# Optimization experiments

Hardware: AMD Instinct MI355X
Metric: run time of the kernel (lower is better)

## Reference

```python
import jax, jax.numpy as jnp
import numpy as np

K = 1024          # num_embeddings (static for segment_sum)
D = 256           # embedding_dim
B, H, W = 32, 64, 64
DECAY = 0.99
EPS = 1e-05
BETA = 0.25


def setup_inputs() -> dict:
    key = jax.random.key(0)
    k1, k2 = jax.random.split(key)
    z = jax.random.normal(k1, (B, D, H, W), dtype=jnp.float32)
    embedding = jax.random.normal(k2, (K, D), dtype=jnp.float32)
    ema_cluster_size = jnp.zeros((K,), dtype=jnp.float32)
    ema_embedding = embedding.copy()
    return {"z": z, "embedding": embedding,
            "ema_cluster_size": ema_cluster_size,
            "ema_embedding": ema_embedding}


def reference(z, embedding, ema_cluster_size, ema_embedding):
    b, d, h, w = z.shape
    # (B, D, H, W) -> (B*H*W, D)
    z_flat = jnp.transpose(z, (0, 2, 3, 1)).reshape(-1, d)
    # squared L2 distances to each code: ||z||^2 - 2 z.E^T + ||E||^2  -> (N, K)
    dist = (jnp.sum(z_flat * z_flat, axis=1, keepdims=True)
            - 2.0 * (z_flat @ embedding.T)
            + jnp.sum(embedding * embedding, axis=1))
    encoding_indices = jnp.argmin(dist, axis=1)                 # (N,)
    # one-hot @ embedding == gather
    quantized = embedding[encoding_indices]                     # (N, D)
    quantized = jnp.transpose(quantized.reshape(b, h, w, d), (0, 3, 1, 2))
    # EMA buffer updates (encodings.sum(0) and encodings.T @ z_flat as segment sums)
    counts = jax.ops.segment_sum(jnp.ones_like(encoding_indices, dtype=z.dtype),
                                 encoding_indices, num_segments=K)
    dw = jax.ops.segment_sum(z_flat, encoding_indices, num_segments=K)
    new_cluster_size = DECAY * ema_cluster_size + (1.0 - DECAY) * counts
    new_ema_embedding = DECAY * ema_embedding + (1.0 - DECAY) * dw
    # straight-through estimator
    quantized_ste = z + jax.lax.stop_gradient(quantized - z)
    commitment_loss = BETA * jnp.mean(jnp.square(z - jax.lax.stop_gradient(quantized_ste)))
    return (quantized_ste, commitment_loss, encoding_indices,
            new_cluster_size, new_ema_embedding)
```

## Files before the change

### kernel.cpp

```cpp
#include <hip/hip_runtime.h>

#define KC 1024
#define DD 256
#define NP 131072
#define HWSZ 4096
#define TOTZ 33554432

#define OUT_Q    0
#define OUT_LOSS 33554432
#define OUT_IDX  33554433
#define OUT_CS   33685505
#define OUT_EMA  33686529

#define WS_IDX    0
#define WS_COUNTS 131072
#define WS_RCNT   132096
#define WS_LOSSP  132352
#define WS_ENORM  132608
#define WS_RLIST  133632
#define WS_EAUG   264704
#define WS_NEED_FLOATS (WS_EAUG + 393216)

#define MARGIN 0.0625f
#define RTILE 16

typedef __attribute__((ext_vector_type(8))) short bf16x8;
typedef __attribute__((ext_vector_type(4))) float f32x4;

__device__ inline unsigned short f2bf_rne(float x) {
    unsigned u = __float_as_uint(x);
    unsigned r = u + 0x7FFFu + ((u >> 16) & 1u);
    return (unsigned short)(r >> 16);
}
__device__ inline float bf2f(unsigned short h) {
    return __uint_as_float(((unsigned)h) << 16);
}
__device__ inline unsigned long long packkey(float d, int c) {
    unsigned u = __float_as_uint(d);
    u = (u & 0x80000000u) ? ~u : (u | 0x80000000u);
    return (((unsigned long long)u) << 32) | (unsigned)c;
}

__global__ __launch_bounds__(256) void enorm_kernel(const float* __restrict__ emb,
                                                    float* __restrict__ enorm) {
    const int k = blockIdx.x;
    float v = emb[k * DD + threadIdx.x];
    v *= v;
    #pragma unroll
    for (int off = 32; off > 0; off >>= 1) v += __shfl_down(v, off);
    __shared__ float red[4];
    if ((threadIdx.x & 63) == 0) red[threadIdx.x >> 6] = v;
    __syncthreads();
    if (threadIdx.x == 0) enorm[k] = (red[0] + red[1]) + (red[2] + red[3]);
}

__global__ __launch_bounds__(256) void convert_emb_kernel(
    const float* __restrict__ emb, unsigned short* __restrict__ eaug)
{
    const int blk = blockIdx.x;
    const int cc = blk >> 3, ksp = blk & 7;
    const int ks = ksp + ((ksp >= 4) ? 4 : 0);
    const int mode = (ks >= 8);
    unsigned short* outp = eaug + (size_t)(cc * 12 + ks) * 8192;
    #pragma unroll
    for (int i = 0; i < 4; ++i) {
        const int f = i * 256 + threadIdx.x;
        const int kc = f >> 9, nt = (f >> 6) & 7, lane = f & 63;
        const int q = lane >> 4, col = lane & 15;
        const int n = cc * 128 + nt * 16 + col;
        const int k0 = ((ks * 64) & 255) + kc * 32 + q * 8;
        const float* src = emb + (size_t)n * 256 + k0;
        unsigned short v[8];
        #pragma unroll
        for (int j = 0; j < 8; ++j) {
            const float x = src[j];
            const unsigned short h = f2bf_rne(x);
            v[j] = mode ? f2bf_rne(x - bf2f(h)) : h;
        }
        *(uint4*)(outp + (size_t)f * 8) = *(uint4*)v;
    }
}

__global__ __launch_bounds__(512, 2) void gemm_argmin_kernel(
    const float* __restrict__ z, const unsigned short* __restrict__ eaug,
    const float* __restrict__ enorm, int* __restrict__ idx_out,
    float* __restrict__ idx_out_f, float* __restrict__ counts,
    int* __restrict__ rcnt, int* __restrict__ rlist)
{
    __shared__ float smem[39296];
    unsigned short* aS = (unsigned short*)smem;
    float* dumpB = smem + 32768;
    float* dumpS = smem + 32768 + 2176;
    int*   dumpI = (int*)(smem + 32768 + 4352);
    const int t = threadIdx.x, w = t >> 6, lane = t & 63;
    const int q = lane >> 4, col = lane & 15;
    const int pt = blockIdx.x;

    #pragma unroll 2
    for (int jj0 = 0; jj0 < 8; ++jj0) {
        const int jj = jj0 * 512 + t;
        const int kslot = jj >> 10;
        const int r = jj & 1023;
        const int kc = r >> 9, mt = (r >> 6) & 7, lf = r & 63;
        const int qq = lf >> 4, cl = lf & 15;
        const int p = pt * 128 + mt * 16 + cl;
        const int b = p >> 12, hw = p & 4095;
        const int k0 = kslot * 64 + kc * 32 + qq * 8;
        const float* src = z + (size_t)b * 1048576 + (size_t)k0 * 4096 + hw;
        unsigned short vh[8], vm[8];
        #pragma unroll
        for (int i = 0; i < 8; ++i) {
            const float x = src[i * 4096];
            const unsigned short h = f2bf_rne(x);
            vh[i] = h;
            vm[i] = f2bf_rne(x - bf2f(h));
        }
        const int off = kc * 4096 + mt * 512 + lf * 8;
        *(uint4*)(aS + kslot * 8192 + off) = *(uint4*)vh;
        *(uint4*)(aS + (4 + kslot) * 8192 + off) = *(uint4*)vm;
    }
    __syncthreads();

#define MFMA_SET(BREG, KCI)                                                   \
    {                                                                         \
        bf16x8 af[8];                                                         \
        _Pragma("unroll")                                                     \
        for (int mi = 0; mi < 8; ++mi)                                        \
            af[mi] = *(const bf16x8*)(aS + slabH * 8192 + (KCI) * 4096        \
                                      + mi * 512 + lane * 8);                 \
        __builtin_amdgcn_s_setprio(1);                                        \
        _Pragma("unroll")                                                     \
        for (int mi = 0; mi < 8; ++mi)                                        \
            _Pragma("unroll")                                                 \
            for (int ni = 0; ni < 4; ++ni)                                    \
                acc[mi][ni] = __builtin_amdgcn_mfma_f32_16x16x32_bf16(        \
                    af[mi], BREG[ni], acc[mi][ni], 0, 0, 0);                  \
        __builtin_amdgcn_s_setprio(0);                                        \
        if (s < 4) {                                                          \
            _Pragma("unroll")                                                 \
            for (int mi = 0; mi < 8; ++mi)                                    \
                af[mi] = *(const bf16x8*)(aS + (4 + slabH) * 8192             \
                                          + (KCI) * 4096 + mi * 512           \
                                          + lane * 8);                        \
            __builtin_amdgcn_s_setprio(1);                                    \
            _Pragma("unroll")                                                 \
            for (int mi = 0; mi < 8; ++mi)                                    \
                _Pragma("unroll")                                             \
                for (int ni = 0; ni < 4; ++ni)                                \
                    acc[mi][ni] = __builtin_amdgcn_mfma_f32_16x16x32_bf16(    \
                        af[mi], BREG[ni], acc[mi][ni], 0, 0, 0);              \
            __builtin_amdgcn_s_setprio(0);                                    \
        }                                                                     \
    }

    #pragma unroll 1
    for (int g = 0; g < 2; ++g) {
        const int ccg = g * 4 + (w >> 1);
        const int nqh = w & 1;
        const int nbase = g * 512 + w * 64;
        const unsigned short* eb = eaug + (size_t)ccg * 98304 + nqh * 2048
                                 + (size_t)lane * 8;
        float en[4];
        #pragma unroll
        for (int ni = 0; ni < 4; ++ni) en[ni] = enorm[nbase + ni * 16 + col];

        f32x4 acc[8][4];
        #pragma unroll
        for (int mi = 0; mi < 8; ++mi)
            #pragma unroll
            for (int ni = 0; ni < 4; ++ni) acc[mi][ni] = (f32x4){0.f, 0.f, 0.f, 0.f};

        bf16x8 b0[4], b1[4], bn[4];
        #pragma unroll
        for (int ni = 0; ni < 4; ++ni) b0[ni] = *(const bf16x8*)(eb + ni * 512);

        #pragma unroll 1
        for (int s = 0; s < 8; ++s) {
            const int ksE = (s < 4) ? s : (4 + s);
            const int slabH = (s < 4) ? s : (s - 4);
            #pragma unroll
            for (int ni = 0; ni < 4; ++ni)
                b1[ni] = *(const bf16x8*)(eb + ksE * 8192 + 4096 + ni * 512);
            if (s < 7) {
                const int ksN = (s < 3) ? (s + 1) : ((s == 3) ? 8 : (5 + s));
                #pragma unroll
                for (int ni = 0; ni < 4; ++ni)
                    bn[ni] = *(const bf16x8*)(eb + ksN * 8192 + ni * 512);
            } else if (g == 0) {
                const unsigned short* eb1 = eaug + (size_t)(4 + (w >> 1)) * 98304
                                          + nqh * 2048 + (size_t)lane * 8;
                #pragma unroll
                for (int ni = 0; ni < 4; ++ni)
                    bn[ni] = *(const bf16x8*)(eb1 + ni * 512);
            }
            MFMA_SET(b0, 0)
            MFMA_SET(b1, 1)
            if (s < 7 || g == 0) {
                #pragma unroll
                for (int ni = 0; ni < 4; ++ni) b0[ni] = bn[ni];
            }
        }

        #pragma unroll
        for (int mi = 0; mi < 8; ++mi) {
            #pragma unroll
            for (int r = 0; r < 4; ++r) {
                float v0 = fmaf(-2.f, acc[mi][0][r], en[0]);
                float v1 = fmaf(-2.f, acc[mi][1][r], en[1]);
                float v2 = fmaf(-2.f, acc[mi][2][r], en[2]);
                float v3 = fmaf(-2.f, acc[mi][3][r], en[3]);
                const int nb = nbase + col;
                float b01 = fminf(v0, v1), x01 = fmaxf(v0, v1);
                int   i01 = (v1 < v0) ? nb + 16 : nb;
                float b23 = fminf(v2, v3), x23 = fmaxf(v2, v3);
                int   i23 = (v3 < v2) ? nb + 48 : nb + 32;
                float b = fminf(b01, b23);
                int   ib = (b23 < b01) ? i23 : i01;
                float s2 = fminf(fmaxf(b01, b23), fminf(x01, x23));
                #pragma unroll
                for (int m = 1; m < 16; m <<= 1) {
                    const float ob = __shfl_xor(b, m);
                    const float os = __shfl_xor(s2, m);
                    const int   oi = __shfl_xor(ib, m);
                    const bool sw = ob < b;
                    const float cand = sw ? b : ob;
                    const float osel = sw ? os : s2;
                    b  = sw ? ob : b;
                    ib = sw ? oi : ib;
                    s2 = fminf(cand, osel);
                }
                if (col == 0) {
                    const int pl = mi * 16 + q * 4 + r;
                    const int e = w * 2 + g;
                    dumpB[pl * 17 + e] = b;
                    dumpS[pl * 17 + e] = s2;
                    dumpI[pl * 17 + e] = ib;
                }
            }
        }
    }
#undef MFMA_SET

    __syncthreads();
    if (t < 128) {
        float B = 3.4e38f, S = 3.4e38f; int I = 0;
        #pragma unroll
        for (int e = 0; e < 16; ++e) {
            const float b = dumpB[t * 17 + e];
            const float s2 = dumpS[t * 17 + e];
            const int   i = dumpI[t * 17 + e];
            if (b < B) { S = fminf(B, s2); B = b; I = i; }
            else       { S = fminf(S, b); }
        }
        const int p = pt * 128 + t;
        idx_out[p] = I;
        idx_out_f[p] = (float)I;
        atomicAdd(&counts[I], 1.0f);
        if (S - B < MARGIN) {
            const int pos = atomicAdd(rcnt, 1);
            rlist[pos] = p;
        }
    }
}

__global__ __launch_bounds__(256) void rescue_kernel(
    const float* __restrict__ z, const float* __restrict__ emb,
    const float* __restrict__ enorm, const int* __restrict__ rcnt,
    const int* __restrict__ rlist, int* __restrict__ idx_out,
    float* __restrict__ idx_out_f, float* __restrict__ counts)
{
    __shared__ float zl[RTILE][DD];
    __shared__ unsigned long long lkey[RTILE];
    const int n = *rcnt;
    if (n <= 0) return;
    const int ntiles = (n + RTILE - 1) / RTILE;
    const int t = threadIdx.x;
    const int slot = t & 15, drow = t >> 4;
    #pragma unroll 1
    for (int tile = blockIdx.x; tile < ntiles; tile += gridDim.x) {
        const int base = tile * RTILE;
        {
            const int ridx = min(base + slot, n - 1);
            const int p = rlist[ridx];
            const int b = p >> 12, hw = p & 4095;
            const float* zp = z + (size_t)b * 1048576 + hw;
            #pragma unroll
            for (int j = 0; j < 16; ++j)
                zl[slot][drow * 16 + j] = zp[(size_t)(drow * 16 + j) * 4096];
        }
        if (t < RTILE) lkey[t] = ~0ull;
        __syncthreads();
        float dot[RTILE][4];
        #pragma unroll
        for (int p = 0; p < RTILE; ++p)
            #pragma unroll
            for (int ci = 0; ci < 4; ++ci) dot[p][ci] = 0.f;
        #pragma unroll 1
        for (int d4 = 0; d4 < 64; ++d4) {
            float4 ev[4];
            #pragma unroll
            for (int ci = 0; ci < 4; ++ci)
                ev[ci] = *(const float4*)(emb + (size_t)(ci * 256 + t) * 256 + d4 * 4);
            #pragma unroll
            for (int p = 0; p < RTILE; ++p) {
                const float4 zv = *(const float4*)(&zl[p][d4 * 4]);
                #pragma unroll
                for (int ci = 0; ci < 4; ++ci) {
                    dot[p][ci] = fmaf(zv.x, ev[ci].x, dot[p][ci]);
                    dot[p][ci] = fmaf(zv.y, ev[ci].y, dot[p][ci]);
                    dot[p][ci] = fmaf(zv.z, ev[ci].z, dot[p][ci]);
                    dot[p][ci] = fmaf(zv.w, ev[ci].w, dot[p][ci]);
                }
            }
        }
        float en[4];
        #pragma unroll
        for (int ci = 0; ci < 4; ++ci) en[ci] = enorm[ci * 256 + t];
        #pragma unroll
        for (int p = 0; p < RTILE; ++p) {
            unsigned long long k = packkey(fmaf(-2.f, dot[p][0], en[0]), t);
            #pragma unroll
            for (int ci = 1; ci < 4; ++ci) {
                const unsigned long long k2 =
                    packkey(fmaf(-2.f, dot[p][ci], en[ci]), ci * 256 + t);
                k = (k2 < k) ? k2 : k;
            }
            atomicMin(&lkey[p], k);
        }
        __syncthreads();
        if (t < RTILE && base + t < n) {
            const int p = rlist[base + t];
            const int fc = (int)(lkey[t] & 0xFFFFFFFFull);
            const int old = idx_out[p];
            if (fc != old) {
                atomicAdd(&counts[old], -1.0f);
                atomicAdd(&counts[fc], 1.0f);
                idx_out[p] = fc;
                idx_out_f[p] = (float)fc;
            }
        }
        __syncthreads();
    }
}

__global__ __launch_bounds__(512) void dwq_kernel(
    const float* __restrict__ z, const float* __restrict__ emb,
    const int* __restrict__ idx, const float* __restrict__ ema_emb,
    float* __restrict__ out_q, float* __restrict__ out_ema,
    float* __restrict__ lossp)
{
    __shared__ float kdw[2][KC];
    __shared__ float ecol[KC];
    __shared__ float red[8];
    const int d = blockIdx.x;
    const int t = threadIdx.x;
    #pragma unroll
    for (int k = t; k < KC; k += 512) {
        kdw[0][k] = 0.f; kdw[1][k] = 0.f;
        ecol[k] = emb[(size_t)k * 256 + d];
    }
    __syncthreads();
    float* kd = kdw[t & 1];
    float ls = 0.f;
    #pragma unroll 1
    for (int it = 0; it < 64; ++it) {
        const int e = it * 512 + t;
        const int b = e >> 10, hwi = (e & 1023) << 2;
        const size_t zoff = (size_t)b * 1048576 + (size_t)d * 4096 + hwi;
        const float4 zv = *(const float4*)(z + zoff);
        const int4 iv = *(const int4*)(idx + b * 4096 + hwi);
        const float q0 = ecol[iv.x], q1 = ecol[iv.y], q2 = ecol[iv.z], q3 = ecol[iv.w];
        float4 qv; qv.x = q0; qv.y = q1; qv.z = q2; qv.w = q3;
        *(float4*)(out_q + zoff) = qv;
        atomicAdd(&kd[iv.x], zv.x);
        atomicAdd(&kd[iv.y], zv.y);
        atomicAdd(&kd[iv.z], zv.z);
        atomicAdd(&kd[iv.w], zv.w);
        const float d0 = zv.x - q0, d1 = zv.y - q1, d2 = zv.z - q2, d3 = zv.w - q3;
        ls += (d0 * d0 + d1 * d1) + (d2 * d2 + d3 * d3);
    }
    __syncthreads();
    #pragma unroll
    for (int k = t; k < KC; k += 512)
        out_ema[(size_t)k * 256 + d] = 0.99f * ema_emb[(size_t)k * 256 + d]
                                     + 0.01f * (kdw[0][k] + kdw[1][k]);
    #pragma unroll
    for (int off = 32; off > 0; off >>= 1) ls += __shfl_down(ls, off);
    if ((t & 63) == 0) red[t >> 6] = ls;
    __syncthreads();
    if (t == 0) {
        float s = 0.f;
        #pragma unroll
        for (int i = 0; i < 8; ++i) s += red[i];
        lossp[blockIdx.x] = s;
    }
}

__global__ __launch_bounds__(256) void finalize_kernel(
    const float* __restrict__ ema_cs, const float* __restrict__ counts,
    const float* __restrict__ lossp, float* __restrict__ out)
{
    const int i = blockIdx.x * 256 + threadIdx.x;
    out[OUT_CS + i] = 0.99f * ema_cs[i] + 0.01f * counts[i];
    if (blockIdx.x == 0) {
        float s = lossp[threadIdx.x];
        #pragma unroll
        for (int off = 32; off > 0; off >>= 1) s += __shfl_down(s, off);
        __shared__ float red[4];
        if ((threadIdx.x & 63) == 0) red[threadIdx.x >> 6] = s;
        __syncthreads();
        if (threadIdx.x == 0)
            out[OUT_LOSS] = 0.25f * ((red[0] + red[1]) + (red[2] + red[3])) / 33554432.0f;
    }
}

__global__ __launch_bounds__(256) void dist_argmin_kernel(
    const float* __restrict__ z, const float* __restrict__ emb,
    const float* __restrict__ enorm, int* __restrict__ idx_out,
    float* __restrict__ idx_out_f, float* __restrict__ counts)
{
    __shared__ float smem[4096];
    float* As = smem;
    float* Bs = smem + 1024;
    const int tid = threadIdx.x;
    const int tx = tid & 15, ty = tid >> 4;
    const int p0 = blockIdx.x * 128;
    const int b = p0 >> 12, hw0 = p0 & 4095;
    const float* zb = z + (size_t)b * (DD * HWSZ) + hw0;
    const int arow = (tid & 31) * 4, akd = tid >> 5;
    const int bcode = tid >> 1, bj = (tid & 1) * 4;
    float best[8]; int bidx[8];
    #pragma unroll
    for (int i = 0; i < 8; i++) { best[i] = 3.4e38f; bidx[i] = 0; }
    #pragma unroll 1
    for (int cc = 0; cc < 8; ++cc) {
        const int c0 = cc * 128;
        float acc[8][8];
        #pragma unroll
        for (int i = 0; i < 8; i++)
            #pragma unroll
            for (int j = 0; j < 8; j++) acc[i][j] = 0.0f;
        #pragma unroll 1
        for (int dk = 0; dk < 32; ++dk) {
            const int kk0 = dk * 8;
            const float4 av = *(const float4*)(zb + (kk0 + akd) * HWSZ + arow);
            const float4 bv = *(const float4*)(emb + (c0 + bcode) * DD + kk0 + bj);
            __syncthreads();
            *(float4*)(As + akd * 128 + arow) = av;
            Bs[(bj + 0) * 128 + bcode] = bv.x;
            Bs[(bj + 1) * 128 + bcode] = bv.y;
            Bs[(bj + 2) * 128 + bcode] = bv.z;
            Bs[(bj + 3) * 128 + bcode] = bv.w;
            __syncthreads();
            #pragma unroll
            for (int kk = 0; kk < 8; ++kk) {
                const float4 a0 = *(const float4*)(As + kk * 128 + ty * 8);
                const float4 a1 = *(const float4*)(As + kk * 128 + ty * 8 + 4);
                const float4 b0 = *(const float4*)(Bs + kk * 128 + tx * 8);
                const float4 b1 = *(const float4*)(Bs + kk * 128 + tx * 8 + 4);
                const float a[8] = {a0.x,a0.y,a0.z,a0.w,a1.x,a1.y,a1.z,a1.w};
                const float bb[8] = {b0.x,b0.y,b0.z,b0.w,b1.x,b1.y,b1.z,b1.w};
                #pragma unroll
                for (int i = 0; i < 8; i++)
                    #pragma unroll
                    for (int j = 0; j < 8; j++)
                        acc[i][j] = fmaf(a[i], bb[j], acc[i][j]);
            }
        }
        const float4 en0 = *(const float4*)(enorm + c0 + tx * 8);
        const float4 en1 = *(const float4*)(enorm + c0 + tx * 8 + 4);
        const float en[8] = {en0.x,en0.y,en0.z,en0.w,en1.x,en1.y,en1.z,en1.w};
        #pragma unroll
        for (int j = 0; j < 8; j++) {
            const int c = c0 + tx * 8 + j;
            #pragma unroll
            for (int i = 0; i < 8; i++) {
                const float dist = fmaf(-2.0f, acc[i][j], en[j]);
                if (dist < best[i]) { best[i] = dist; bidx[i] = c; }
            }
        }
    }
    __syncthreads();
    float* rmin = smem;
    int* ridx = (int*)(smem + 2048);
    #pragma unroll
    for (int i = 0; i < 8; i++) {
        const int r = ty * 8 + i;
        rmin[r * 16 + tx] = best[i];
        ridx[r * 16 + tx] = bidx[i];
    }
    __syncthreads();
    if (tid < 128) {
        const int r = tid;
        float m = rmin[r * 16]; int mi = ridx[r * 16];
        #pragma unroll
        for (int tt = 1; tt < 16; tt++) {
            const float v = rmin[r * 16 + tt];
            const int vi = ridx[r * 16 + tt];
            if (v < m || (v == m && vi < mi)) { m = v; mi = vi; }
        }
        const int p = p0 + r;
        idx_out[p] = mi;
        idx_out_f[p] = (float)mi;
        atomicAdd(&counts[mi], 1.0f);
    }
}

extern "C" void kernel_launch(void* const* d_in, const int* in_sizes, int n_in,
                              void* d_out, int out_size, void* d_ws, size_t ws_size,
                              hipStream_t stream) {
    const float* z       = (const float*)d_in[0];
    const float* emb     = (const float*)d_in[1];
    const float* ema_cs  = (const float*)d_in[2];
    const float* ema_emb = (const float*)d_in[3];
    float* out = (float*)d_out;
    float* ws  = (float*)d_ws;

    int*   ws_idx    = (int*)(ws + WS_IDX);
    float* ws_counts = ws + WS_COUNTS;
    int*   ws_rcnt   = (int*)(ws + WS_RCNT);
    float* ws_lossp  = ws + WS_LOSSP;
    float* ws_enorm  = ws + WS_ENORM;
    int*   ws_rlist  = (int*)(ws + WS_RLIST);
    unsigned short* ws_eaug = (unsigned short*)(ws + WS_EAUG);

    hipMemsetAsync(ws_counts, 0, 1025 * sizeof(float), stream);
    hipLaunchKernelGGL(enorm_kernel, dim3(KC), dim3(256), 0, stream, emb, ws_enorm);

    if (ws_size >= (size_t)WS_NEED_FLOATS * sizeof(float)) {
        hipLaunchKernelGGL(convert_emb_kernel, dim3(64), dim3(256), 0, stream, emb, ws_eaug);
        hipLaunchKernelGGL(gemm_argmin_kernel, dim3(1024), dim3(512), 0, stream,
                           z, ws_eaug, ws_enorm, ws_idx, out + OUT_IDX,
                           ws_counts, ws_rcnt, ws_rlist);
        hipLaunchKernelGGL(rescue_kernel, dim3(512), dim3(256), 0, stream,
                           z, emb, ws_enorm, ws_rcnt, ws_rlist,
                           ws_idx, out + OUT_IDX, ws_counts);
    } else {
        hipLaunchKernelGGL(dist_argmin_kernel, dim3(NP / 128), dim3(256), 0, stream,
                           z, emb, ws_enorm, ws_idx, out + OUT_IDX, ws_counts);
    }

    hipLaunchKernelGGL(dwq_kernel, dim3(DD), dim3(512), 0, stream,
                       z, emb, ws_idx, ema_emb, out, out + OUT_EMA, ws_lossp);
    hipLaunchKernelGGL(finalize_kernel, dim3(4), dim3(256), 0, stream,
                       ema_cs, ws_counts, ws_lossp, out);
}
```

Baseline: 741.7 us.

## Split GEMM-argmin work over 16 waves with per-wave code slices and row halves

The distance GEMM + argmin kernel now runs 1024-thread blocks. Each of the 16 waves owns a fixed 64-code slice across both row halves, instead of 8 waves each covering 128 rows and two code groups. The per-wave accumulator tile is halved, which reduces register pressure and doubles resident waves to hide MFMA and LDS latency. The argmin shuffle reduction is shortened and a cross-wave reduction runs per row half. The cost is reloading embedding fragments for each row half, extra block-wide barriers, and tighter launch bounds that may cause spills.

```diff
diff --git a/kernel.cpp b/kernel.cpp
--- a/kernel.cpp
+++ b/kernel.cpp
@@ -81,24 +81,24 @@
     }
 }
 
-__global__ __launch_bounds__(512, 2) void gemm_argmin_kernel(
+__global__ __launch_bounds__(1024, 4) void gemm_argmin_kernel(
     const float* __restrict__ z, const unsigned short* __restrict__ eaug,
     const float* __restrict__ enorm, int* __restrict__ idx_out,
     float* __restrict__ idx_out_f, float* __restrict__ counts,
     int* __restrict__ rcnt, int* __restrict__ rlist)
 {
-    __shared__ float smem[39296];
+    __shared__ float smem[38912];
     unsigned short* aS = (unsigned short*)smem;
-    float* dumpB = smem + 32768;
-    float* dumpS = smem + 32768 + 2176;
-    int*   dumpI = (int*)(smem + 32768 + 4352);
+    float* dB = smem + 32768;
+    float* dS = smem + 32768 + 2048;
+    int*   dI = (int*)(smem + 32768 + 4096);
     const int t = threadIdx.x, w = t >> 6, lane = t & 63;
     const int q = lane >> 4, col = lane & 15;
     const int pt = blockIdx.x;
 
-    #pragma unroll 2
-    for (int jj0 = 0; jj0 < 8; ++jj0) {
-        const int jj = jj0 * 512 + t;
+    #pragma unroll
+    for (int jj0 = 0; jj0 < 4; ++jj0) {
+        const int jj = jj0 * 1024 + t;
         const int kslot = jj >> 10;
         const int r = jj & 1023;
         const int kc = r >> 9, mt = (r >> 6) & 7, lf = r & 63;
@@ -121,16 +121,19 @@
     }
     __syncthreads();
 
-#define MFMA_SET(BREG, KCI)                                                   \
+    const unsigned short* eb = eaug + (size_t)(w >> 1) * 98304
+                             + (w & 1) * 2048 + (size_t)lane * 8;
+
+#define COMPUTE_SET(BREG, KCI)                                                \
     {                                                                         \
-        bf16x8 af[8];                                                         \
+        bf16x8 af[4];                                                         \
         _Pragma("unroll")                                                     \
-        for (int mi = 0; mi < 8; ++mi)                                        \
+        for (int mi = 0; mi < 4; ++mi)                                        \
             af[mi] = *(const bf16x8*)(aS + slabH * 8192 + (KCI) * 4096        \
-                                      + mi * 512 + lane * 8);                 \
+                                      + (g4 + mi) * 512 + lane * 8);          \
         __builtin_amdgcn_s_setprio(1);                                        \
         _Pragma("unroll")                                                     \
-        for (int mi = 0; mi < 8; ++mi)                                        \
+        for (int mi = 0; mi < 4; ++mi)                                        \
             _Pragma("unroll")                                                 \
             for (int ni = 0; ni < 4; ++ni)                                    \
                 acc[mi][ni] = __builtin_amdgcn_mfma_f32_16x16x32_bf16(        \
@@ -138,13 +141,13 @@
         __builtin_amdgcn_s_setprio(0);                                        \
         if (s < 4) {                                                          \
             _Pragma("unroll")                                                 \
-            for (int mi = 0; mi < 8; ++mi)                                    \
+            for (int mi = 0; mi < 4; ++mi)                                    \
                 af[mi] = *(const bf16x8*)(aS + (4 + slabH) * 8192             \
-                                          + (KCI) * 4096 + mi * 512           \
+                                          + (KCI) * 4096 + (g4 + mi) * 512    \
                                           + lane * 8);                        \
             __builtin_amdgcn_s_setprio(1);                                    \
             _Pragma("unroll")                                                 \
-            for (int mi = 0; mi < 8; ++mi)                                    \
+            for (int mi = 0; mi < 4; ++mi)                                    \
                 _Pragma("unroll")                                             \
                 for (int ni = 0; ni < 4; ++ni)                                \
                     acc[mi][ni] = __builtin_amdgcn_mfma_f32_16x16x32_bf16(    \
@@ -155,61 +158,49 @@
 
     #pragma unroll 1
     for (int g = 0; g < 2; ++g) {
-        const int ccg = g * 4 + (w >> 1);
-        const int nqh = w & 1;
-        const int nbase = g * 512 + w * 64;
-        const unsigned short* eb = eaug + (size_t)ccg * 98304 + nqh * 2048
-                                 + (size_t)lane * 8;
-        float en[4];
-        #pragma unroll
-        for (int ni = 0; ni < 4; ++ni) en[ni] = enorm[nbase + ni * 16 + col];
-
-        f32x4 acc[8][4];
-        #pragma unroll
-        for (int mi = 0; mi < 8; ++mi)
+        const int g4 = g * 4;
+        f32x4 acc[4][4];
+        #pragma unroll
+        for (int mi = 0; mi < 4; ++mi)
             #pragma unroll
             for (int ni = 0; ni < 4; ++ni) acc[mi][ni] = (f32x4){0.f, 0.f, 0.f, 0.f};
 
-        bf16x8 b0[4], b1[4], bn[4];
-        #pragma unroll
-        for (int ni = 0; ni < 4; ++ni) b0[ni] = *(const bf16x8*)(eb + ni * 512);
+        bf16x8 bA[4], bB[4];
+        #pragma unroll
+        for (int ni = 0; ni < 4; ++ni)
+            bA[ni] = *(const bf16x8*)(eb + ni * 512);
 
         #pragma unroll 1
         for (int s = 0; s < 8; ++s) {
             const int ksE = (s < 4) ? s : (4 + s);
-            const int slabH = (s < 4) ? s : (s - 4);
+            const int slabH = s & 3;
             #pragma unroll
             for (int ni = 0; ni < 4; ++ni)
-                b1[ni] = *(const bf16x8*)(eb + ksE * 8192 + 4096 + ni * 512);
+                bB[ni] = *(const bf16x8*)(eb + ksE * 8192 + 4096 + ni * 512);
+            COMPUTE_SET(bA, 0)
             if (s < 7) {
-                const int ksN = (s < 3) ? (s + 1) : ((s == 3) ? 8 : (5 + s));
+                const int ksN = (s < 3) ? (s + 1) : ((s == 3) ? 8 : (s + 5));
                 #pragma unroll
                 for (int ni = 0; ni < 4; ++ni)
-                    bn[ni] = *(const bf16x8*)(eb + ksN * 8192 + ni * 512);
-            } else if (g == 0) {
-                const unsigned short* eb1 = eaug + (size_t)(4 + (w >> 1)) * 98304
-                                          + nqh * 2048 + (size_t)lane * 8;
-                #pragma unroll
-                for (int ni = 0; ni < 4; ++ni)
-                    bn[ni] = *(const bf16x8*)(eb1 + ni * 512);
-            }
-            MFMA_SET(b0, 0)
-            MFMA_SET(b1, 1)
-            if (s < 7 || g == 0) {
-                #pragma unroll
-                for (int ni = 0; ni < 4; ++ni) b0[ni] = bn[ni];
-            }
-        }
-
-        #pragma unroll
-        for (int mi = 0; mi < 8; ++mi) {
+                    bA[ni] = *(const bf16x8*)(eb + ksN * 8192 + ni * 512);
+            }
+            COMPUTE_SET(bB, 1)
+        }
+
+        const int wbase = w * 64;
+        #pragma unroll
+        for (int mi = 0; mi < 4; ++mi) {
             #pragma unroll
             for (int r = 0; r < 4; ++r) {
-                float v0 = fmaf(-2.f, acc[mi][0][r], en[0]);
-                float v1 = fmaf(-2.f, acc[mi][1][r], en[1]);
-                float v2 = fmaf(-2.f, acc[mi][2][r], en[2]);
-                float v3 = fmaf(-2.f, acc[mi][3][r], en[3]);
-                const int nb = nbase + col;
+                const float en0 = enorm[wbase + col];
+                const float en1 = enorm[wbase + 16 + col];
+                const float en2 = enorm[wbase + 32 + col];
+                const float en3 = enorm[wbase + 48 + col];
+                float v0 = fmaf(-2.f, acc[mi][0][r], en0);
+                float v1 = fmaf(-2.f, acc[mi][1][r], en1);
+                float v2 = fmaf(-2.f, acc[mi][2][r], en2);
+                float v3 = fmaf(-2.f, acc[mi][3][r], en3);
+                const int nb = wbase + col;
                 float b01 = fminf(v0, v1), x01 = fmaxf(v0, v1);
                 int   i01 = (v1 < v0) ? nb + 16 : nb;
                 float b23 = fminf(v2, v3), x23 = fmaxf(v2, v3);
@@ -218,7 +209,7 @@
                 int   ib = (b23 < b01) ? i23 : i01;
                 float s2 = fminf(fmaxf(b01, b23), fminf(x01, x23));
                 #pragma unroll
-                for (int m = 1; m < 16; m <<= 1) {
+                for (int m = 1; m < 8; m <<= 1) {
                     const float ob = __shfl_xor(b, m);
                     const float os = __shfl_xor(s2, m);
                     const int   oi = __shfl_xor(ib, m);
@@ -229,38 +220,42 @@
                     ib = sw ? oi : ib;
                     s2 = fminf(cand, osel);
                 }
-                if (col == 0) {
-                    const int pl = mi * 16 + q * 4 + r;
-                    const int e = w * 2 + g;
-                    dumpB[pl * 17 + e] = b;
-                    dumpS[pl * 17 + e] = s2;
-                    dumpI[pl * 17 + e] = ib;
+                if ((col & 7) == 0) {
+                    const int slot = mi * 4 + r;
+                    const int di = w * 128 + slot * 8 + q * 2 + (col >> 3);
+                    dB[di] = b; dS[di] = s2; dI[di] = ib;
                 }
             }
         }
-    }
-#undef MFMA_SET
-
-    __syncthreads();
-    if (t < 128) {
-        float B = 3.4e38f, S = 3.4e38f; int I = 0;
-        #pragma unroll
-        for (int e = 0; e < 16; ++e) {
-            const float b = dumpB[t * 17 + e];
-            const float s2 = dumpS[t * 17 + e];
-            const int   i = dumpI[t * 17 + e];
-            if (b < B) { S = fminf(B, s2); B = b; I = i; }
-            else       { S = fminf(S, b); }
-        }
-        const int p = pt * 128 + t;
-        idx_out[p] = I;
-        idx_out_f[p] = (float)I;
-        atomicAdd(&counts[I], 1.0f);
-        if (S - B < MARGIN) {
-            const int pos = atomicAdd(rcnt, 1);
-            rlist[pos] = p;
-        }
-    }
+        __syncthreads();
+        if (t < 64) {
+            const int mi = t >> 4, qq = (t >> 2) & 3, rr = t & 3;
+            const int slot = mi * 4 + rr;
+            float B = 3.4e38f, S = 3.4e38f; int I = 0;
+            #pragma unroll
+            for (int wv = 0; wv < 16; ++wv) {
+                #pragma unroll
+                for (int h = 0; h < 2; ++h) {
+                    const int di = wv * 128 + slot * 8 + qq * 2 + h;
+                    const float b = dB[di];
+                    const float s2 = dS[di];
+                    const int   i = dI[di];
+                    if (b < B) { S = fminf(B, s2); B = b; I = i; }
+                    else       { S = fminf(S, b); }
+                }
+            }
+            const int p = pt * 128 + g * 64 + t;
+            idx_out[p] = I;
+            idx_out_f[p] = (float)I;
+            atomicAdd(&counts[I], 1.0f);
+            if (S - B < MARGIN) {
+                const int pos = atomicAdd(rcnt, 1);
+                rlist[pos] = p;
+            }
+        }
+        __syncthreads();
+    }
+#undef COMPUTE_SET
 }
 
 __global__ __launch_bounds__(256) void rescue_kernel(
@@ -529,7 +524,7 @@
 
     if (ws_size >= (size_t)WS_NEED_FLOATS * sizeof(float)) {
         hipLaunchKernelGGL(convert_emb_kernel, dim3(64), dim3(256), 0, stream, emb, ws_eaug);
-        hipLaunchKernelGGL(gemm_argmin_kernel, dim3(1024), dim3(512), 0, stream,
+        hipLaunchKernelGGL(gemm_argmin_kernel, dim3(1024), dim3(1024), 0, stream,
                            z, ws_eaug, ws_enorm, ws_idx, out + OUT_IDX,
                            ws_counts, ws_rcnt, ws_rlist);
         hipLaunchKernelGGL(rescue_kernel, dim3(512), dim3(256), 0, stream,
```

Result: slower. 1.038 ms (+39.9%).
